# Optimization experiments

Measured on AMD Instinct MI355X. Metric: run time of the kernel, lower is better.

Reference implementation:

```python
import jax, jax.numpy as jnp
import numpy as np

N_HEADS = 16
ROPE_BASE = 10000.0


def _rotate_half(x):
    d = x.shape[-1] // 2
    return jnp.concatenate([-x[..., d:], x[..., :d]], axis=-1)


def _rope_tables(L, head_dim, dtype):
    inv_freq = 1.0 / (ROPE_BASE ** (jnp.arange(0, head_dim, 2, dtype=jnp.float32) / head_dim))
    t = jnp.arange(L, dtype=jnp.float32)
    freqs = jnp.outer(t, inv_freq)  # [L, head_dim//2]
    # torch code repeats cos/sin along last dim (tile x2) -> concat([c, c])
    cos = jnp.concatenate([jnp.cos(freqs), jnp.cos(freqs)], axis=-1).astype(dtype)
    sin = jnp.concatenate([jnp.sin(freqs), jnp.sin(freqs)], axis=-1).astype(dtype)
    return cos[None, None], sin[None, None]  # [1,1,L,head_dim]


def setup_inputs() -> dict:
    key = jax.random.key(0)
    kx, kq, kk, kv, ko = jax.random.split(key, 5)
    B, L, D = 4, 2048, 1024
    s = 0.02
    return {
        "x": jax.random.normal(kx, (B, L, D), dtype=jnp.float32),
        "Wq": jax.random.normal(kq, (D, D), dtype=jnp.float32) * s,
        "Wk": jax.random.normal(kk, (D, D), dtype=jnp.float32) * s,
        "Wv": jax.random.normal(kv, (D, D), dtype=jnp.float32) * s,
        "Wo": jax.random.normal(ko, (D, D), dtype=jnp.float32) * s,
    }


def reference(x, Wq, Wk, Wv, Wo):
    B, L, D = x.shape
    H = N_HEADS
    hd = D // H

    def split_heads(y):
        return y.reshape(B, L, H, hd).transpose(0, 2, 1, 3)  # [B,H,L,hd]

    q = split_heads(x @ Wq.T)
    k = split_heads(x @ Wk.T)
    v = split_heads(x @ Wv.T)

    cos, sin = _rope_tables(L, hd, x.dtype)
    q = q * cos + _rotate_half(q) * sin
    k = k * cos + _rotate_half(k) * sin

    scale = 1.0 / jnp.sqrt(jnp.asarray(hd, dtype=x.dtype))
    scores = jnp.einsum("bhqd,bhkd->bhqk", q, k) * scale
    attn = jax.nn.softmax(scores, axis=-1)
    out = jnp.einsum("bhqk,bhkd->bhqd", attn, v)
    out = out.transpose(0, 2, 1, 3).reshape(B, L, D)
    return out @ Wo.T
```

## Files before the change

### kernel.cpp

```cpp
#include <hip/hip_runtime.h>


typedef __bf16 bf16_t;
typedef __bf16 bf16x8 __attribute__((ext_vector_type(8)));
typedef __bf16 bf16x4 __attribute__((ext_vector_type(4)));
typedef float  floatx4 __attribute__((ext_vector_type(4)));
typedef unsigned int u32x2 __attribute__((ext_vector_type(2)));

#define B_  4
#define L_  2048
#define D_  1024
#define H_  16
#define HD_ 64
#define M_  (B_*L_)

__device__ __forceinline__ void async_copy16(const bf16_t* g, bf16_t* l) {
  __builtin_amdgcn_global_load_lds(
      (const __attribute__((address_space(1))) void*)g,
      (__attribute__((address_space(3))) void*)l, 16, 0, 0);
}

__device__ __forceinline__ unsigned int pack_bf16(float a, float b) {
  unsigned short ua = __builtin_bit_cast(unsigned short, (bf16_t)a);
  unsigned short ub = __builtin_bit_cast(unsigned short, (bf16_t)b);
  return (unsigned int)ua | ((unsigned int)ub << 16);
}

__device__ __forceinline__ unsigned int cvt_pk(float lo, float hi) {
  unsigned int r;
  asm("v_cvt_pk_bf16_f32 %0, %1, %2" : "=v"(r) : "v"(lo), "v"(hi));
  return r;
}

__global__ void prep_kernel(const float* __restrict__ x,
                            const float* __restrict__ wq, const float* __restrict__ wk,
                            const float* __restrict__ wv, const float* __restrict__ wo,
                            bf16_t* __restrict__ xb,
                            bf16_t* __restrict__ wqb, bf16_t* __restrict__ wkb,
                            bf16_t* __restrict__ wvb, bf16_t* __restrict__ wob,
                            float* __restrict__ cosT, float* __restrict__ sinT)
{
  const int NXv = (M_*D_) >> 3;
  const int NWv = (D_*D_) >> 3;
  const int NC  = NXv + 4*NWv;
  int i = blockIdx.x*256 + threadIdx.x;
  if (i < NC) {
    const float* s; bf16_t* d; size_t o;
    if (i < NXv) { s = x; d = xb; o = (size_t)i << 3; }
    else {
      int r = i - NXv; int w = r >> 17;
      o = (size_t)(r & (NWv-1)) << 3;
      s = (w==0)?wq:(w==1)?wk:(w==2)?wv:wo;
      d = (w==0)?wqb:(w==1)?wkb:(w==2)?wvb:wob;
    }
    float4 a = *(const float4*)(s+o);
    float4 b = *(const float4*)(s+o+4);
    bf16x8 v;
    v[0]=(bf16_t)a.x; v[1]=(bf16_t)a.y; v[2]=(bf16_t)a.z; v[3]=(bf16_t)a.w;
    v[4]=(bf16_t)b.x; v[5]=(bf16_t)b.y; v[6]=(bf16_t)b.z; v[7]=(bf16_t)b.w;
    *(bf16x8*)(d+o) = v;
    return;
  }
  i -= NC;
  if (i < L_*32) {
    int f = i >> 11, l = i & 2047;
    double inv = pow(10000.0, -(double)f / 32.0);
    double ang = (double)l * inv;
    cosT[i] = (float)cos(ang);
    sinT[i] = (float)sin(ang);
  }
}

template<int MODE>
__global__ __launch_bounds__(256) void gemm_kernel(
    const bf16_t* __restrict__ A,
    const bf16_t* __restrict__ W0, const bf16_t* __restrict__ W1, const bf16_t* __restrict__ W2,
    bf16_t* __restrict__ C0, bf16_t* __restrict__ C1, bf16_t* __restrict__ C2,
    float* __restrict__ Cf,
    const float* __restrict__ cosT, const float* __restrict__ sinT)
{
  __shared__ __align__(16) bf16_t Sh[16384];
  bf16_t* As = Sh;
  bf16_t* Bs = Sh + 8192;
  const int KD = 1024, ND = 1024;
  int z = (MODE==0) ? (int)blockIdx.z : 0;
  const bf16_t* W = (MODE==1) ? W0 : (z==0 ? W0 : (z==1 ? W1 : W2));
  int m0 = blockIdx.x*128, n0 = blockIdx.y*128;
  int tid = threadIdx.x;
  int wave = tid>>6, lane = tid&63, quad = lane>>4, lr = lane&15;
  int wm = wave>>1, wn = wave&1;
  int srow = lane>>3, sslot = lane&7;

  floatx4 zero4 = {0.f,0.f,0.f,0.f};
  floatx4 acc[4][4];
  #pragma unroll
  for (int i=0;i<4;i++)
    #pragma unroll
    for (int j=0;j<4;j++) acc[i][j] = zero4;

  #pragma unroll 1
  for (int k0 = 0; k0 < KD; k0 += 64) {
    #pragma unroll
    for (int j=0;j<4;j++) {
      int chunk = wave + j*4;
      int row = chunk*8 + srow;
      int col = ((sslot ^ (row&7)) << 3);
      async_copy16(A + (size_t)(m0+row)*KD + k0 + col, &As[chunk*512]);
      async_copy16(W + (size_t)(n0+row)*KD + k0 + col, &Bs[chunk*512]);
    }
    __syncthreads();
    #pragma unroll
    for (int ks=0; ks<2; ks++) {
      bf16x8 af[4], bfr[4];
      #pragma unroll
      for (int mi=0;mi<4;mi++)
        af[mi] = *(const bf16x8*)&As[(wm*64+mi*16+lr)*64 + (((ks*4+quad) ^ (lr&7))<<3)];
      #pragma unroll
      for (int ni=0;ni<4;ni++)
        bfr[ni] = *(const bf16x8*)&Bs[(wn*64+ni*16+lr)*64 + (((ks*4+quad) ^ (lr&7))<<3)];
      #pragma unroll
      for (int mi=0;mi<4;mi++)
        #pragma unroll
        for (int ni=0;ni<4;ni++)
          acc[mi][ni] = __builtin_amdgcn_mfma_f32_16x16x32_bf16(af[mi], bfr[ni], acc[mi][ni], 0,0,0);
    }
    __syncthreads();
  }

  if (MODE==1) {
    #pragma unroll
    for (int mi=0;mi<4;mi++) {
      int row = m0 + wm*64 + mi*16 + quad*4;
      #pragma unroll
      for (int ni=0;ni<4;ni++) {
        int col = n0 + wn*64 + ni*16 + lr;
        #pragma unroll
        for (int r=0;r<4;r++)
          Cf[(size_t)(row+r)*ND + col] = acc[mi][ni][r];
      }
    }
  } else if (z < 2) {
    bf16_t* Cb = (z==0) ? C0 : C1;
    const float sc = (z==0) ? 0.18033688011112042f : 1.0f;
    #pragma unroll
    for (int mi=0;mi<4;mi++) {
      int row = m0 + wm*64 + mi*16 + quad*4;
      int l = row & 2047;
      #pragma unroll
      for (int ni=0;ni<2;ni++) {
        int col = n0 + wn*64 + ni*16 + lr;
        int f = ni*16 + lr;
        float4 cv = *(const float4*)&cosT[f*2048 + l];
        float4 sv = *(const float4*)&sinT[f*2048 + l];
        #pragma unroll
        for (int r=0;r<4;r++) {
          float c = (&cv.x)[r];
          float s = (&sv.x)[r];
          float lo = acc[mi][ni][r], hi = acc[mi][ni+2][r];
          Cb[(size_t)(row+r)*ND + col]      = (bf16_t)((lo*c - hi*s)*sc);
          Cb[(size_t)(row+r)*ND + col + 32] = (bf16_t)((hi*c + lo*s)*sc);
        }
      }
    }
  } else {
    #pragma unroll
    for (int mi=0;mi<4;mi++) {
      int rowm = wm*64 + mi*16 + quad*4;
      #pragma unroll
      for (int ni=0;ni<4;ni++) {
        int coln = wn*64 + ni*16 + lr;
        uint2 val;
        val.x = pack_bf16(acc[mi][ni][0], acc[mi][ni][1]);
        val.y = pack_bf16(acc[mi][ni][2], acc[mi][ni][3]);
        *(uint2*)&Sh[coln*128 + (rowm ^ ((coln&15)<<3))] = val;
      }
    }
    __syncthreads();
    int bb = m0 >> 11, l0 = m0 & 2047;
    #pragma unroll
    for (int rep=0; rep<8; rep++) {
      int idx = rep*256 + tid;
      int coln = idx >> 4, seg = idx & 15;
      bf16x8 v = *(const bf16x8*)&Sh[coln*128 + ((seg*8) ^ ((coln&15)<<3))];
      int cg = n0 + coln;
      *(bf16x8*)&C2[((size_t)((bb<<4) + (cg>>6))*64 + (cg&63))*2048 + l0 + seg*8] = v;
    }
  }
}

__global__ __launch_bounds__(256) void attn_kernel(
    const bf16_t* __restrict__ Q, const bf16_t* __restrict__ K,
    const bf16_t* __restrict__ Vt, bf16_t* __restrict__ O)
{
  __shared__ __align__(16) bf16_t Ks[3][4096];
  __shared__ __align__(16) bf16_t Vs[3][4096];
  int tid = threadIdx.x;
  int wave = tid>>6, lane = tid&63, quad = lane>>4, lr = lane&15;
  int bh = blockIdx.x; int b = bh>>4, h = bh&15;
  int q0 = blockIdx.y*128 + wave*32;
  size_t rowQ = (size_t)b*L_ + q0;

  int slr = (lr&3) | ((lr&4)<<1) | ((lr&8)>>1);
  int srow8 = lane>>3;
  int sslot = lane&7;

  bf16x8 qf[2][2];
  #pragma unroll
  for (int n=0;n<2;n++)
    #pragma unroll
    for (int ks=0;ks<2;ks++)
      qf[n][ks] = *(const bf16x8*)&Q[(rowQ + n*16 + lr)*D_ + h*HD_ + ks*32 + quad*8];

  const bf16_t* Kg = K + (size_t)b*L_*D_ + h*HD_;
  const bf16_t* Vg = Vt + (size_t)bh*HD_*L_;

  bf16x8 onesf;
  #pragma unroll
  for (int j=0;j<8;j++) onesf[j] = (bf16_t)1.0f;

  floatx4 zero4 = {0.f,0.f,0.f,0.f};
  floatx4 accO[2][4];
  floatx4 accS[2];
  accS[0] = zero4; accS[1] = zero4;
  #pragma unroll
  for (int n=0;n<2;n++)
    #pragma unroll
    for (int dt=0;dt<4;dt++) accO[n][dt] = zero4;

  floatx4 StA[2][4], StB[2][4];

  auto stage = [&](int it, int c) {
    #pragma unroll
    for (int j=0;j<2;j++) {
      int row = wave*16 + j*8 + srow8;
      int col = ((sslot ^ (row&7)) << 3);
      async_copy16(Kg + (size_t)(it*64 + row)*D_ + col, &Ks[c][(wave*16 + j*8)*64]);
      async_copy16(Vg + (size_t)row*L_ + it*64 + col,   &Vs[c][(wave*16 + j*8)*64]);
    }
  };

  stage(0, 0);
  stage(1, 1);
  asm volatile("s_waitcnt vmcnt(0)" ::: "memory");
  __builtin_amdgcn_s_barrier();

#define QKT_M(CN, SN)                                                         \
    _Pragma("unroll")                                                         \
    for (int t=0;t<4;t++) { SN[0][t]=zero4; SN[1][t]=zero4; }                 \
    _Pragma("unroll")                                                         \
    for (int t=0;t<4;t++) {                                                   \
      _Pragma("unroll")                                                       \
      for (int ks=0;ks<2;ks++) {                                              \
        bf16x8 kf = *(const bf16x8*)&Ks[CN][(t*16+slr)*64 + (((ks*4+quad) ^ (slr&7))<<3)]; \
        SN[0][t] = __builtin_amdgcn_mfma_f32_16x16x32_bf16(kf, qf[0][ks], SN[0][t], 0,0,0); \
        SN[1][t] = __builtin_amdgcn_mfma_f32_16x16x32_bf16(kf, qf[1][ks], SN[1][t], 0,0,0); \
      }                                                                       \
    }

  QKT_M(0, StA)

#define ATTN_BODY(IT, CC, SC, SN, DO_STAGE, DO_QKT, DO_SYNC)                  \
  {                                                                           \
    if (DO_STAGE) stage((IT)+2, ((CC)+2)%3);                                  \
    bf16x8 pfv[2][2];                                                         \
    _Pragma("unroll")                                                         \
    for (int n=0;n<2;n++) {                                                   \
      _Pragma("unroll")                                                       \
      for (int hh=0;hh<2;hh++) {                                              \
        unsigned int w00 = cvt_pk(exp2f(SC[n][2*hh][0]),   exp2f(SC[n][2*hh][1]));   \
        unsigned int w01 = cvt_pk(exp2f(SC[n][2*hh][2]),   exp2f(SC[n][2*hh][3]));   \
        unsigned int w10 = cvt_pk(exp2f(SC[n][2*hh+1][0]), exp2f(SC[n][2*hh+1][1])); \
        unsigned int w11 = cvt_pk(exp2f(SC[n][2*hh+1][2]), exp2f(SC[n][2*hh+1][3])); \
        u32x2 r0 = __builtin_amdgcn_permlane32_swap(w00, w10, false, false);  \
        u32x2 r1 = __builtin_amdgcn_permlane32_swap(w01, w11, false, false);  \
        union { unsigned int u[4]; bf16x8 v; } pu;                            \
        pu.u[0] = r0.x; pu.u[1] = r1.x; pu.u[2] = r0.y; pu.u[3] = r1.y;       \
        pfv[n][hh] = pu.v;                                                    \
      }                                                                       \
    }                                                                         \
    if (DO_QKT) { QKT_M(((CC)+1)%3, SN) }                                     \
    _Pragma("unroll")                                                         \
    for (int dt=0;dt<4;dt++) {                                                \
      _Pragma("unroll")                                                       \
      for (int hh=0;hh<2;hh++) {                                              \
        bf16x8 vf = *(const bf16x8*)&Vs[CC][(dt*16+lr)*64 + (((hh*4+quad) ^ (lr&7))<<3)]; \
        accO[0][dt] = __builtin_amdgcn_mfma_f32_16x16x32_bf16(vf, pfv[0][hh], accO[0][dt], 0,0,0); \
        accO[1][dt] = __builtin_amdgcn_mfma_f32_16x16x32_bf16(vf, pfv[1][hh], accO[1][dt], 0,0,0); \
      }                                                                       \
    }                                                                         \
    accS[0] = __builtin_amdgcn_mfma_f32_16x16x32_bf16(onesf, pfv[0][0], accS[0], 0,0,0); \
    accS[1] = __builtin_amdgcn_mfma_f32_16x16x32_bf16(onesf, pfv[1][0], accS[1], 0,0,0); \
    accS[0] = __builtin_amdgcn_mfma_f32_16x16x32_bf16(onesf, pfv[0][1], accS[0], 0,0,0); \
    accS[1] = __builtin_amdgcn_mfma_f32_16x16x32_bf16(onesf, pfv[1][1], accS[1], 0,0,0); \
    if (DO_SYNC) {                                                            \
      asm volatile("s_waitcnt vmcnt(0)" ::: "memory");                        \
      __builtin_amdgcn_s_barrier();                                           \
    }                                                                         \
  }

  #pragma unroll 1
  for (int itb = 0; itb < 30; itb += 6) {
    ATTN_BODY(itb+0, 0, StA, StB, true, true, true);
    ATTN_BODY(itb+1, 1, StB, StA, true, true, true);
    ATTN_BODY(itb+2, 2, StA, StB, true, true, true);
    ATTN_BODY(itb+3, 0, StB, StA, true, true, true);
    ATTN_BODY(itb+4, 1, StA, StB, true, true, true);
    ATTN_BODY(itb+5, 2, StB, StA, true, true, true);
  }
  ATTN_BODY(30, 0, StA, StB, false, true,  false);
  ATTN_BODY(31, 1, StB, StA, false, false, false);
#undef ATTN_BODY
#undef QKT_M

  float inv0 = 1.0f / accS[0][0];
  float inv1 = 1.0f / accS[1][0];
  #pragma unroll
  for (int n=0;n<2;n++) {
    float inv = n ? inv1 : inv0;
    #pragma unroll
    for (int dt=0;dt<4;dt++) {
      uint2 w;
      w.x = cvt_pk(accO[n][dt][0]*inv, accO[n][dt][1]*inv);
      w.y = cvt_pk(accO[n][dt][2]*inv, accO[n][dt][3]*inv);
      *(uint2*)&O[(rowQ + n*16 + lr)*D_ + h*HD_ + dt*16 + quad*4] = w;
    }
  }
}

extern "C" void kernel_launch(void* const* d_in, const int* in_sizes, int n_in,
                              void* d_out, int out_size, void* d_ws, size_t ws_size,
                              hipStream_t stream) {
  const float* x  = (const float*)d_in[0];
  const float* wq = (const float*)d_in[1];
  const float* wk = (const float*)d_in[2];
  const float* wv = (const float*)d_in[3];
  const float* wo = (const float*)d_in[4];

  char* ws = (char*)d_ws;
  bf16_t* xb  = (bf16_t*)(ws);
  bf16_t* Qb  = (bf16_t*)(ws + (size_t)(16u<<20));
  bf16_t* Kb  = (bf16_t*)(ws + (size_t)(32u<<20));
  bf16_t* Vtb = (bf16_t*)(ws + (size_t)(48u<<20));
  bf16_t* wqb = (bf16_t*)(ws + (size_t)(64u<<20));
  bf16_t* wkb = (bf16_t*)(ws + (size_t)(66u<<20));
  bf16_t* wvb = (bf16_t*)(ws + (size_t)(68u<<20));
  bf16_t* wob = (bf16_t*)(ws + (size_t)(70u<<20));
  float* cosT = (float*)(ws + (size_t)(72u<<20));
  float* sinT = (float*)(ws + (size_t)(72u<<20) + (256u<<10));
  bf16_t* Ob = xb;

  prep_kernel<<<6400, 256, 0, stream>>>(x, wq, wk, wv, wo, xb, wqb, wkb, wvb, wob, cosT, sinT);
  gemm_kernel<0><<<dim3(64,8,3), 256, 0, stream>>>(xb, wqb, wkb, wvb, Qb, Kb, Vtb, nullptr, cosT, sinT);
  attn_kernel<<<dim3(64,16), 256, 0, stream>>>(Qb, Kb, Vtb, Ob);
  gemm_kernel<1><<<dim3(64,8,1), 256, 0, stream>>>(Ob, wob, nullptr, nullptr,
                                                   nullptr, nullptr, nullptr, (float*)d_out, cosT, sinT);
}
```

Baseline: 288.9 us.

## Double-buffer GEMM k-loop and simplify attention pipeline to two stages

```diff
diff --git a/kernel.cpp b/kernel.cpp
--- a/kernel.cpp
+++ b/kernel.cpp
@@ -80,8 +80,6 @@
     const float* __restrict__ cosT, const float* __restrict__ sinT)
 {
   __shared__ __align__(16) bf16_t Sh[16384];
-  bf16_t* As = Sh;
-  bf16_t* Bs = Sh + 8192;
   const int KD = 1024, ND = 1024;
   int z = (MODE==0) ? (int)blockIdx.z : 0;
   const bf16_t* W = (MODE==1) ? W0 : (z==0 ? W0 : (z==1 ? W1 : W2));
@@ -89,7 +87,11 @@
   int tid = threadIdx.x;
   int wave = tid>>6, lane = tid&63, quad = lane>>4, lr = lane&15;
   int wm = wave>>1, wn = wave&1;
-  int srow = lane>>3, sslot = lane&7;
+
+  int g16 = lane>>2;
+  int skey = ((lane>>3)&3) ^ ((lane>>5)&1);
+  int scol = (((lane&3) ^ skey) << 3);
+  int rkey = ((lr>>1)&3) ^ ((lr>>3)&1);
 
   floatx4 zero4 = {0.f,0.f,0.f,0.f};
   floatx4 acc[4][4];
@@ -98,34 +100,47 @@
     #pragma unroll
     for (int j=0;j<4;j++) acc[i][j] = zero4;
 
+  auto stageA = [&](int ts, int cb, int j) {
+    int ch = wave + j*4;
+    int grow = ch*16 + g16;
+    async_copy16(A + (size_t)(m0+grow)*KD + ts*32 + scol, &Sh[cb*4096 + ch*512]);
+  };
+  auto stageB = [&](int ts, int cb, int j) {
+    int ch = wave + j*4;
+    int grow = ch*16 + g16;
+    async_copy16(W + (size_t)(n0+grow)*KD + ts*32 + scol, &Sh[8192 + cb*4096 + ch*512]);
+  };
+
+  stageA(0,0,0); stageA(0,0,1); stageB(0,0,0); stageB(0,0,1);
+  __syncthreads();
+
+#define GBODY(T, CB, DO_STAGE)                                                \
+  {                                                                           \
+    if (DO_STAGE) {                                                           \
+      stageA((T)+1, (CB)^1, 0); stageA((T)+1, (CB)^1, 1);                     \
+      stageB((T)+1, (CB)^1, 0); stageB((T)+1, (CB)^1, 1);                     \
+    }                                                                         \
+    bf16x8 af[4], bfr[4];                                                     \
+    _Pragma("unroll")                                                         \
+    for (int mi=0;mi<4;mi++)                                                  \
+      af[mi]  = *(const bf16x8*)&Sh[(CB)*4096 + (wm*64+mi*16+lr)*32 + ((quad^rkey)<<3)]; \
+    _Pragma("unroll")                                                         \
+    for (int ni=0;ni<4;ni++)                                                  \
+      bfr[ni] = *(const bf16x8*)&Sh[8192 + (CB)*4096 + (wn*64+ni*16+lr)*32 + ((quad^rkey)<<3)]; \
+    _Pragma("unroll")                                                         \
+    for (int mi=0;mi<4;mi++)                                                  \
+      _Pragma("unroll")                                                       \
+      for (int ni=0;ni<4;ni++)                                                \
+        acc[mi][ni] = __builtin_amdgcn_mfma_f32_16x16x32_bf16(af[mi], bfr[ni], acc[mi][ni], 0,0,0); \
+    __syncthreads();                                                          \
+  }
+
   #pragma unroll 1
-  for (int k0 = 0; k0 < KD; k0 += 64) {
-    #pragma unroll
-    for (int j=0;j<4;j++) {
-      int chunk = wave + j*4;
-      int row = chunk*8 + srow;
-      int col = ((sslot ^ (row&7)) << 3);
-      async_copy16(A + (size_t)(m0+row)*KD + k0 + col, &As[chunk*512]);
-      async_copy16(W + (size_t)(n0+row)*KD + k0 + col, &Bs[chunk*512]);
-    }
-    __syncthreads();
-    #pragma unroll
-    for (int ks=0; ks<2; ks++) {
-      bf16x8 af[4], bfr[4];
-      #pragma unroll
-      for (int mi=0;mi<4;mi++)
-        af[mi] = *(const bf16x8*)&As[(wm*64+mi*16+lr)*64 + (((ks*4+quad) ^ (lr&7))<<3)];
-      #pragma unroll
-      for (int ni=0;ni<4;ni++)
-        bfr[ni] = *(const bf16x8*)&Bs[(wn*64+ni*16+lr)*64 + (((ks*4+quad) ^ (lr&7))<<3)];
-      #pragma unroll
-      for (int mi=0;mi<4;mi++)
-        #pragma unroll
-        for (int ni=0;ni<4;ni++)
-          acc[mi][ni] = __builtin_amdgcn_mfma_f32_16x16x32_bf16(af[mi], bfr[ni], acc[mi][ni], 0,0,0);
-    }
-    __syncthreads();
-  }
+  for (int t2 = 0; t2 < 32; t2 += 2) {
+    GBODY(t2,   0, true);
+    GBODY(t2+1, 1, (t2+2 < 32));
+  }
+#undef GBODY
 
   if (MODE==1) {
     #pragma unroll
@@ -192,8 +207,8 @@
     const bf16_t* __restrict__ Q, const bf16_t* __restrict__ K,
     const bf16_t* __restrict__ Vt, bf16_t* __restrict__ O)
 {
-  __shared__ __align__(16) bf16_t Ks[3][4096];
-  __shared__ __align__(16) bf16_t Vs[3][4096];
+  __shared__ __align__(16) bf16_t Ks[2][4096];
+  __shared__ __align__(16) bf16_t Vs[2][4096];
   int tid = threadIdx.x;
   int wave = tid>>6, lane = tid&63, quad = lane>>4, lr = lane&15;
   int bh = blockIdx.x; int b = bh>>4, h = bh&15;
@@ -227,8 +242,6 @@
     #pragma unroll
     for (int dt=0;dt<4;dt++) accO[n][dt] = zero4;
 
-  floatx4 StA[2][4], StB[2][4];
-
   auto stage = [&](int it, int c) {
     #pragma unroll
     for (int j=0;j<2;j++) {
@@ -240,37 +253,33 @@
   };
 
   stage(0, 0);
-  stage(1, 1);
   asm volatile("s_waitcnt vmcnt(0)" ::: "memory");
   __builtin_amdgcn_s_barrier();
 
-#define QKT_M(CN, SN)                                                         \
-    _Pragma("unroll")                                                         \
-    for (int t=0;t<4;t++) { SN[0][t]=zero4; SN[1][t]=zero4; }                 \
+#define ATTN_BODY(IT, CC, DO_STAGE)                                           \
+  {                                                                           \
+    if (DO_STAGE) stage((IT)+1, (CC)^1);                                      \
+    floatx4 St[2][4];                                                         \
+    _Pragma("unroll")                                                         \
+    for (int t=0;t<4;t++) { St[0][t]=zero4; St[1][t]=zero4; }                 \
     _Pragma("unroll")                                                         \
     for (int t=0;t<4;t++) {                                                   \
       _Pragma("unroll")                                                       \
       for (int ks=0;ks<2;ks++) {                                              \
-        bf16x8 kf = *(const bf16x8*)&Ks[CN][(t*16+slr)*64 + (((ks*4+quad) ^ (slr&7))<<3)]; \
-        SN[0][t] = __builtin_amdgcn_mfma_f32_16x16x32_bf16(kf, qf[0][ks], SN[0][t], 0,0,0); \
-        SN[1][t] = __builtin_amdgcn_mfma_f32_16x16x32_bf16(kf, qf[1][ks], SN[1][t], 0,0,0); \
+        bf16x8 kf = *(const bf16x8*)&Ks[CC][(t*16+slr)*64 + (((ks*4+quad) ^ (slr&7))<<3)]; \
+        St[0][t] = __builtin_amdgcn_mfma_f32_16x16x32_bf16(kf, qf[0][ks], St[0][t], 0,0,0); \
+        St[1][t] = __builtin_amdgcn_mfma_f32_16x16x32_bf16(kf, qf[1][ks], St[1][t], 0,0,0); \
       }                                                                       \
-    }
-
-  QKT_M(0, StA)
-
-#define ATTN_BODY(IT, CC, SC, SN, DO_STAGE, DO_QKT, DO_SYNC)                  \
-  {                                                                           \
-    if (DO_STAGE) stage((IT)+2, ((CC)+2)%3);                                  \
+    }                                                                         \
     bf16x8 pfv[2][2];                                                         \
     _Pragma("unroll")                                                         \
     for (int n=0;n<2;n++) {                                                   \
       _Pragma("unroll")                                                       \
       for (int hh=0;hh<2;hh++) {                                              \
-        unsigned int w00 = cvt_pk(exp2f(SC[n][2*hh][0]),   exp2f(SC[n][2*hh][1]));   \
-        unsigned int w01 = cvt_pk(exp2f(SC[n][2*hh][2]),   exp2f(SC[n][2*hh][3]));   \
-        unsigned int w10 = cvt_pk(exp2f(SC[n][2*hh+1][0]), exp2f(SC[n][2*hh+1][1])); \
-        unsigned int w11 = cvt_pk(exp2f(SC[n][2*hh+1][2]), exp2f(SC[n][2*hh+1][3])); \
+        unsigned int w00 = cvt_pk(exp2f(St[n][2*hh][0]),   exp2f(St[n][2*hh][1]));   \
+        unsigned int w01 = cvt_pk(exp2f(St[n][2*hh][2]),   exp2f(St[n][2*hh][3]));   \
+        unsigned int w10 = cvt_pk(exp2f(St[n][2*hh+1][0]), exp2f(St[n][2*hh+1][1])); \
+        unsigned int w11 = cvt_pk(exp2f(St[n][2*hh+1][2]), exp2f(St[n][2*hh+1][3])); \
         u32x2 r0 = __builtin_amdgcn_permlane32_swap(w00, w10, false, false);  \
         u32x2 r1 = __builtin_amdgcn_permlane32_swap(w01, w11, false, false);  \
         union { unsigned int u[4]; bf16x8 v; } pu;                            \
@@ -278,7 +287,6 @@
         pfv[n][hh] = pu.v;                                                    \
       }                                                                       \
     }                                                                         \
-    if (DO_QKT) { QKT_M(((CC)+1)%3, SN) }                                     \
     _Pragma("unroll")                                                         \
     for (int dt=0;dt<4;dt++) {                                                \
       _Pragma("unroll")                                                       \
@@ -292,25 +300,16 @@
     accS[1] = __builtin_amdgcn_mfma_f32_16x16x32_bf16(onesf, pfv[1][0], accS[1], 0,0,0); \
     accS[0] = __builtin_amdgcn_mfma_f32_16x16x32_bf16(onesf, pfv[0][1], accS[0], 0,0,0); \
     accS[1] = __builtin_amdgcn_mfma_f32_16x16x32_bf16(onesf, pfv[1][1], accS[1], 0,0,0); \
-    if (DO_SYNC) {                                                            \
-      asm volatile("s_waitcnt vmcnt(0)" ::: "memory");                        \
-      __builtin_amdgcn_s_barrier();                                           \
-    }                                                                         \
+    asm volatile("s_waitcnt vmcnt(0)" ::: "memory");                          \
+    __builtin_amdgcn_s_barrier();                                             \
   }
 
   #pragma unroll 1
-  for (int itb = 0; itb < 30; itb += 6) {
-    ATTN_BODY(itb+0, 0, StA, StB, true, true, true);
-    ATTN_BODY(itb+1, 1, StB, StA, true, true, true);
-    ATTN_BODY(itb+2, 2, StA, StB, true, true, true);
-    ATTN_BODY(itb+3, 0, StB, StA, true, true, true);
-    ATTN_BODY(itb+4, 1, StA, StB, true, true, true);
-    ATTN_BODY(itb+5, 2, StB, StA, true, true, true);
-  }
-  ATTN_BODY(30, 0, StA, StB, false, true,  false);
-  ATTN_BODY(31, 1, StB, StA, false, false, false);
+  for (int itb = 0; itb < 32; itb += 2) {
+    ATTN_BODY(itb,   0, true);
+    ATTN_BODY(itb+1, 1, (itb+2 < 32));
+  }
 #undef ATTN_BODY
-#undef QKT_M
 
   float inv0 = 1.0f / accS[0][0];
   float inv1 = 1.0f / accS[1][0];
```

Result: slower. 302.9 us (+4.9%).
